# Kernel optimization log

Hardware: AMD Instinct MI355X
Metric: run time of the kernel (lower is better)

## Reference

```python
import jax, jax.numpy as jnp
import numpy as np

B, H, W, C = 4, 56, 56, 128
HEADS, KS, DEPTH, DEPTH_CROSS = 4, 7, 2, 2
HID = 4 * C
EPS = 1e-5


def layer_norm(x, g, b):
    m = jnp.mean(x, axis=-1, keepdims=True)
    v = jnp.mean((x - m) ** 2, axis=-1, keepdims=True)
    return (x - m) * jax.lax.rsqrt(v + EPS) * g + b


def _nbr_idx(L, k):
    # clamped sliding-window start (NATTEN semantics)
    s = np.clip(np.arange(L) - k // 2, 0, L - k)
    n = s[:, None] + np.arange(k)            # [L,k] neighbor coords
    r = n - np.arange(L)[:, None] + (k - 1)  # [L,k] rpb index in [0, 2k-2]
    return jnp.asarray(n), jnp.asarray(r)


def neighborhood_attention(q, kx, vx, rpb):
    # q,kx,vx: [B,h,H,W,d]; rpb: [h,2k-1,2k-1]
    b, h, hh, ww, d = q.shape
    k = KS
    ni, ri = _nbr_idx(hh, k)
    nj, rj = _nbr_idx(ww, k)
    q = q * (d ** -0.5)

    def gather(t):
        t = jnp.take(t, ni.reshape(-1), axis=2).reshape(b, h, hh, k, ww, d)
        t = jnp.take(t, nj.reshape(-1), axis=4).reshape(b, h, hh, k, ww, k, d)
        return t.transpose(0, 1, 2, 4, 3, 5, 6)  # [B,h,H,W,k,k,d]

    kn = gather(kx)
    vn = gather(vx)
    attn = jnp.einsum('bnhwd,bnhwijd->bnhwij', q, kn)
    bias = rpb[:, ri][:, :, :, rj]          # [h,H,k,W,k]
    bias = bias.transpose(0, 1, 3, 2, 4)     # [h,H,W,k,k]
    attn = attn + bias[None]
    attn = jax.nn.softmax(attn.reshape(b, h, hh, ww, k * k), axis=-1)
    out = jnp.einsum('bnhwm,bnhwmd->bnhwd', attn,
                     vn.reshape(b, h, hh, ww, k * k, d))
    return out.transpose(0, 2, 3, 1, 4).reshape(b, hh, ww, h * d)


def mlp(x, f1w, f1b, f2w, f2b):
    return jax.nn.gelu(x @ f1w + f1b, approximate=False) @ f2w + f2b


def sa_layer(x, n1g, n1b, qkvw, qkvb, rpb, pw, pb, n2g, n2b, f1w, f1b, f2w, f2b):
    b, hh, ww, c = x.shape
    d = c // HEADS
    hn = layer_norm(x, n1g, n1b)
    qkv = (hn @ qkvw + qkvb).reshape(b, hh, ww, 3, HEADS, d).transpose(3, 0, 4, 1, 2, 5)
    a = neighborhood_attention(qkv[0], qkv[1], qkv[2], rpb) @ pw + pb
    x = x + a
    x = x + mlp(layer_norm(x, n2g, n2b), f1w, f1b, f2w, f2b)
    return x


def cross_layer(x_multi, q_in, n1g, n1b, qw, qb, kvw, kvb, rpb, pw, pb,
                n2g, n2b, f1w, f1b, f2w, f2b):
    b, hh, ww, c = x_multi.shape
    d = c // HEADS
    hn = layer_norm(x_multi, n1g, n1b)
    q = (q_in @ qw + qb).reshape(b, hh, ww, HEADS, d).transpose(0, 3, 1, 2, 4)
    kv = (hn @ kvw + kvb).reshape(b, hh, ww, 2, HEADS, d).transpose(3, 0, 4, 1, 2, 5)
    a = neighborhood_attention(q, kv[0], kv[1], rpb) @ pw + pb
    x = x_multi + a
    x = x + mlp(layer_norm(x, n2g, n2b), f1w, f1b, f2w, f2b)
    return x


def setup_inputs() -> dict:
    key = jax.random.key(0)
    ks = iter(jax.random.split(key, 64))

    def nrm(shape, s=0.02):
        return (jax.random.normal(next(ks), shape, dtype=jnp.float32) * s)

    D, Dc = DEPTH, DEPTH_CROSS
    inp = {
        'x': jax.random.normal(next(ks), (B, H, W, C), dtype=jnp.float32),
        'x_multi': jax.random.normal(next(ks), (B, H, W, C), dtype=jnp.float32),
        # self-attention NATLayers (stacked over depth)
        'sa_n1g': jnp.ones((D, C), jnp.float32), 'sa_n1b': jnp.zeros((D, C), jnp.float32),
        'sa_qkv_w': nrm((D, C, 3 * C)), 'sa_qkv_b': jnp.zeros((D, 3 * C), jnp.float32),
        'sa_rpb': nrm((D, HEADS, 2 * KS - 1, 2 * KS - 1)),
        'sa_proj_w': nrm((D, C, C)), 'sa_proj_b': jnp.zeros((D, C), jnp.float32),
        'sa_n2g': jnp.ones((D, C), jnp.float32), 'sa_n2b': jnp.zeros((D, C), jnp.float32),
        'sa_fc1_w': nrm((D, C, HID)), 'sa_fc1_b': jnp.zeros((D, HID), jnp.float32),
        'sa_fc2_w': nrm((D, HID, C)), 'sa_fc2_b': jnp.zeros((D, C), jnp.float32),
        # cross NATCrossLayers (stacked over depth_cross)
        'cr_n1g': jnp.ones((Dc, C), jnp.float32), 'cr_n1b': jnp.zeros((Dc, C), jnp.float32),
        'cr_q_w': nrm((Dc, C, C)), 'cr_q_b': jnp.zeros((Dc, C), jnp.float32),
        'cr_kv_w': nrm((Dc, C, 2 * C)), 'cr_kv_b': jnp.zeros((Dc, 2 * C), jnp.float32),
        'cr_rpb': nrm((Dc, HEADS, 2 * KS - 1, 2 * KS - 1)),
        'cr_proj_w': nrm((Dc, C, C)), 'cr_proj_b': jnp.zeros((Dc, C), jnp.float32),
        'cr_n2g': jnp.ones((Dc, C), jnp.float32), 'cr_n2b': jnp.zeros((Dc, C), jnp.float32),
        'cr_fc1_w': nrm((Dc, C, HID)), 'cr_fc1_b': jnp.zeros((Dc, HID), jnp.float32),
        'cr_fc2_w': nrm((Dc, HID, C)), 'cr_fc2_b': jnp.zeros((Dc, C), jnp.float32),
        # downsample: conv (2C -> 4C, 3x3, stride 2, no bias) + LayerNorm
        'ds_conv_w': nrm((3, 3, 2 * C, 4 * C)),
        'ds_ng': jnp.ones((4 * C,), jnp.float32), 'ds_nb': jnp.zeros((4 * C,), jnp.float32),
    }
    return inp


def reference(x, x_multi,
              sa_n1g, sa_n1b, sa_qkv_w, sa_qkv_b, sa_rpb, sa_proj_w, sa_proj_b,
              sa_n2g, sa_n2b, sa_fc1_w, sa_fc1_b, sa_fc2_w, sa_fc2_b,
              cr_n1g, cr_n1b, cr_q_w, cr_q_b, cr_kv_w, cr_kv_b, cr_rpb,
              cr_proj_w, cr_proj_b, cr_n2g, cr_n2b, cr_fc1_w, cr_fc1_b,
              cr_fc2_w, cr_fc2_b, ds_conv_w, ds_ng, ds_nb):
    x_cross = x
    for i in range(DEPTH):
        x = sa_layer(x, sa_n1g[i], sa_n1b[i], sa_qkv_w[i], sa_qkv_b[i], sa_rpb[i],
                     sa_proj_w[i], sa_proj_b[i], sa_n2g[i], sa_n2b[i],
                     sa_fc1_w[i], sa_fc1_b[i], sa_fc2_w[i], sa_fc2_b[i])
    for i in range(DEPTH_CROSS):
        x_cross = cross_layer(x_multi, x_cross, cr_n1g[i], cr_n1b[i], cr_q_w[i],
                              cr_q_b[i], cr_kv_w[i], cr_kv_b[i], cr_rpb[i],
                              cr_proj_w[i], cr_proj_b[i], cr_n2g[i], cr_n2b[i],
                              cr_fc1_w[i], cr_fc1_b[i], cr_fc2_w[i], cr_fc2_b[i])
    y = jnp.concatenate([x, x_cross], axis=-1)  # [B,H,W,2C]
    y = jax.lax.conv_general_dilated(y, ds_conv_w, (2, 2), [(1, 1), (1, 1)],
                                     dimension_numbers=('NHWC', 'HWIO', 'NHWC'))
    return layer_norm(y, ds_ng, ds_nb)  # [B,H/2,W/2,4C]
```

## Files before the change

kernel.cpp:

```cpp
#include <hip/hip_runtime.h>
#include <math.h>

#define NPIX 12544
#define CH   128
#define HEADS 4
#define HD   32
#define KS   7
#define HID  512
#define HH   56
#define WW   56

typedef __attribute__((ext_vector_type(8))) short bf16x8;
typedef __attribute__((ext_vector_type(4))) float f32x4;
typedef unsigned short u16;

__device__ inline float gelu_f(float x) { return 0.5f * x * (1.0f + erff(x * 0.70710678118654752f)); }

__device__ inline u16 rne_bf16(float x) {
    unsigned u = __float_as_uint(x);
    return (u16)((u + 0x7fffu + ((u >> 16) & 1u)) >> 16);
}
__device__ inline float bf2f(u16 u) {
    return __uint_as_float(((unsigned)u) << 16);
}


template<int MODE>
__device__ __forceinline__ void qln_body(char* sh,
    const float* __restrict__ Af, const u16* __restrict__ Bt,
    const float* __restrict__ lng, const float* __restrict__ lnb,
    const float* __restrict__ bias, u16* __restrict__ Cb,
    int N, int bx, int by)
{
    char* alsb = sh;
    char* blsb = sh + 16384;
    int t = threadIdx.x, lane = t & 63, w = t >> 6;
    int m0 = bx * 64, n0 = by * 64;
    int wr = w >> 1, wc = w & 1;

    {
        int rb = t >> 3, c8 = t & 7;
        float4 va[2][4];
        float sum[2], sq[2];
#pragma unroll
        for (int r2 = 0; r2 < 2; ++r2) {
            int row = r2 * 32 + rb;
            const float4* ap = reinterpret_cast<const float4*>(Af + (size_t)(m0 + row) * 128);
            va[r2][0] = ap[c8 * 2];
            va[r2][1] = ap[c8 * 2 + 1];
            va[r2][2] = ap[16 + c8 * 2];
            va[r2][3] = ap[16 + c8 * 2 + 1];
            float s = 0.f, q = 0.f;
#pragma unroll
            for (int e = 0; e < 4; ++e) {
                float4 x = va[r2][e];
                s += x.x + x.y + x.z + x.w;
                q += x.x * x.x + x.y * x.y + x.z * x.z + x.w * x.w;
            }
            sum[r2] = s; sq[r2] = q;
        }
#pragma unroll
        for (int o = 1; o < 8; o <<= 1) {
            sum[0] += __shfl_xor(sum[0], o); sq[0] += __shfl_xor(sq[0], o);
            sum[1] += __shfl_xor(sum[1], o); sq[1] += __shfl_xor(sq[1], o);
        }
        const float4* gp = reinterpret_cast<const float4*>(lng);
        const float4* bp = reinterpret_cast<const float4*>(lnb);
        float4 g[4], bb[4];
        g[0] = gp[c8 * 2];      g[1] = gp[c8 * 2 + 1];
        g[2] = gp[16 + c8 * 2]; g[3] = gp[16 + c8 * 2 + 1];
        bb[0] = bp[c8 * 2];      bb[1] = bp[c8 * 2 + 1];
        bb[2] = bp[16 + c8 * 2]; bb[3] = bp[16 + c8 * 2 + 1];
#pragma unroll
        for (int r2 = 0; r2 < 2; ++r2) {
            int row = r2 * 32 + rb;
            float mean = sum[r2] * (1.0f / 128.0f);
            float inv = rsqrtf(sq[r2] * (1.0f / 128.0f) - mean * mean + 1e-5f);
#pragma unroll
            for (int h = 0; h < 2; ++h) {
                float4 x0 = va[r2][h * 2], x1 = va[r2][h * 2 + 1];
                float4 g0 = g[h * 2], g1 = g[h * 2 + 1];
                float4 b0 = bb[h * 2], b1 = bb[h * 2 + 1];
                bf16x8 o;
                o[0] = (short)rne_bf16((x0.x - mean) * inv * g0.x + b0.x);
                o[1] = (short)rne_bf16((x0.y - mean) * inv * g0.y + b0.y);
                o[2] = (short)rne_bf16((x0.z - mean) * inv * g0.z + b0.z);
                o[3] = (short)rne_bf16((x0.w - mean) * inv * g0.w + b0.w);
                o[4] = (short)rne_bf16((x1.x - mean) * inv * g1.x + b1.x);
                o[5] = (short)rne_bf16((x1.y - mean) * inv * g1.y + b1.y);
                o[6] = (short)rne_bf16((x1.z - mean) * inv * g1.z + b1.z);
                o[7] = (short)rne_bf16((x1.w - mean) * inv * g1.w + b1.w);
                int byte = (h * 128 + c8 * 16) ^ ((row & 7) << 4);
                *reinterpret_cast<bf16x8*>(alsb + row * 256 + byte) = o;
            }
        }
    }

    f32x4 acc[2][2] = {};
    for (int kk = 0; kk < 2; ++kk) {
#pragma unroll
        for (int i = 0; i < 2; ++i) {
            int s = t + i * 256, row = s >> 3, ch = (s & 7) * 8;
            bf16x8 v = *reinterpret_cast<const bf16x8*>(Bt + (size_t)(n0 + row) * 128 + kk * 64 + ch);
            *reinterpret_cast<bf16x8*>(blsb + row * 128 + ((ch * 2) ^ ((row & 7) << 4))) = v;
        }
        __syncthreads();
#pragma unroll
        for (int sub = 0; sub < 2; ++sub) {
            int kba = (kk * 2 + sub) * 64 + (lane >> 4) * 16;
            int kbb = sub * 64 + (lane >> 4) * 16;
            bf16x8 af[2], bfr[2];
#pragma unroll
            for (int mi = 0; mi < 2; ++mi) {
                int row = wr * 32 + mi * 16 + (lane & 15);
                af[mi] = *reinterpret_cast<const bf16x8*>(alsb + row * 256 + (kba ^ ((row & 7) << 4)));
            }
#pragma unroll
            for (int ni = 0; ni < 2; ++ni) {
                int row = wc * 32 + ni * 16 + (lane & 15);
                bfr[ni] = *reinterpret_cast<const bf16x8*>(blsb + row * 128 + (kbb ^ ((row & 7) << 4)));
            }
#pragma unroll
            for (int mi = 0; mi < 2; ++mi)
#pragma unroll
                for (int ni = 0; ni < 2; ++ni)
                    acc[mi][ni] = __builtin_amdgcn_mfma_f32_16x16x32_bf16(af[mi], bfr[ni], acc[mi][ni], 0, 0, 0);
        }
        __syncthreads();
    }

    int fq = lane >> 4, fr = lane & 15;
#pragma unroll
    for (int mi = 0; mi < 2; ++mi) {
#pragma unroll
        for (int ni = 0; ni < 2; ++ni) {
            int col = n0 + wc * 32 + ni * 16 + fr;
            float bv = bias[col];
#pragma unroll
            for (int j = 0; j < 4; ++j) {
                int row = m0 + wr * 32 + mi * 16 + fq * 4 + j;
                float v = acc[mi][ni][j] + bv;
                if constexpr (MODE == 1) {
                    Cb[(size_t)row * N + col] = rne_bf16(gelu_f(v));
                } else {
                    Cb[(size_t)row * N + col] = rne_bf16(v);
                }
            }
        }
    }
}

template<int MODE>
__device__ __forceinline__ void gemm_body(char* sh,
    const u16* __restrict__ A, const u16* __restrict__ Bt,
    const float* __restrict__ bias, const float* __restrict__ res,
    float* __restrict__ Cf, u16* __restrict__ Cb,
    int N, int K, int bx, int by)
{
    char* alsb = sh;
    char* blsb = sh + 4096;
    int t = threadIdx.x;
    int m0 = bx * 32, n0 = by * 64;
    int lane = t & 63, w = t >> 6;
    int wr = w >> 1, wc = w & 1;
    f32x4 acc[2] = {};
    for (int k0 = 0; k0 < K; k0 += 64) {
        {
            int s = t, row = s >> 3, ch = (s & 7) * 8;
            bf16x8 v = *reinterpret_cast<const bf16x8*>(A + (size_t)(m0 + row) * K + k0 + ch);
            *reinterpret_cast<bf16x8*>(alsb + row * 128 + ((ch * 2) ^ ((row & 7) << 4))) = v;
        }
#pragma unroll
        for (int i = 0; i < 2; ++i) {
            int s = t + i * 256, row = s >> 3, ch = (s & 7) * 8;
            bf16x8 v = *reinterpret_cast<const bf16x8*>(Bt + (size_t)(n0 + row) * K + k0 + ch);
            *reinterpret_cast<bf16x8*>(blsb + row * 128 + ((ch * 2) ^ ((row & 7) << 4))) = v;
        }
        __syncthreads();
#pragma unroll
        for (int kk = 0; kk < 2; ++kk) {
            int kb = kk * 64 + (lane >> 4) * 16;
            int row_a = wr * 16 + (lane & 15);
            bf16x8 af = *reinterpret_cast<const bf16x8*>(alsb + row_a * 128 + (kb ^ ((row_a & 7) << 4)));
#pragma unroll
            for (int ni = 0; ni < 2; ++ni) {
                int row = wc * 32 + ni * 16 + (lane & 15);
                bf16x8 bfr = *reinterpret_cast<const bf16x8*>(blsb + row * 128 + (kb ^ ((row & 7) << 4)));
                acc[ni] = __builtin_amdgcn_mfma_f32_16x16x32_bf16(af, bfr, acc[ni], 0, 0, 0);
            }
        }
        __syncthreads();
    }
    int fq = lane >> 4, fr = lane & 15;
#pragma unroll
    for (int ni = 0; ni < 2; ++ni) {
        int col = n0 + wc * 32 + ni * 16 + fr;
        float bv = bias[col];
#pragma unroll
        for (int j = 0; j < 4; ++j) {
            int row = m0 + wr * 16 + fq * 4 + j;
            float v = acc[ni][j] + bv;
            if constexpr (MODE == 2) {
                Cf[(size_t)row * N + col] = v + res[(size_t)row * N + col];
            } else if constexpr (MODE == 3) {
                Cb[(size_t)row * N + col] = rne_bf16(v);
            } else {
                float r2 = v + res[(size_t)row * N + col];
                Cf[(size_t)row * N + col] = r2;
                Cb[(size_t)row * N + col] = rne_bf16(r2);
            }
        }
    }
}


struct TDesc { const float* src; u16* dst; int K; int N; int tile0; };
struct TPack { TDesc d[19]; };

__global__ __launch_bounds__(256) void prep_kernel(TPack p, int ntile,
    const float* __restrict__ X, float* __restrict__ o1, float* __restrict__ o2,
    u16* __restrict__ ob, int n4)
{
    __shared__ float tl[32][33];
    if ((int)blockIdx.x < ntile) {
        int tile = blockIdx.x;
        int i = 0;
#pragma unroll 1
        while (i < 18 && tile >= p.d[i + 1].tile0) ++i;
        TDesc d = p.d[i];
        int local = tile - d.tile0;
        int ktiles = d.K >> 5;
        int lk = local % ktiles, ln_ = local / ktiles;
        int k0 = lk * 32, n0 = ln_ * 32;
        int tx = threadIdx.x & 31, ty = threadIdx.x >> 5;
#pragma unroll
        for (int r = 0; r < 4; ++r) {
            int row = ty * 4 + r;
            tl[row][tx] = d.src[(size_t)(k0 + row) * d.N + n0 + tx];
        }
        __syncthreads();
#pragma unroll
        for (int r = 0; r < 4; ++r) {
            int row = ty * 4 + r;
            d.dst[(size_t)(n0 + row) * d.K + k0 + tx] = rne_bf16(tl[tx][row]);
        }
    } else {
        int i = ((int)blockIdx.x - ntile) * 256 + threadIdx.x;
        if (i < n4) {
            float4 v = reinterpret_cast<const float4*>(X)[i];
            reinterpret_cast<float4*>(o1)[i] = v;
            reinterpret_cast<float4*>(o2)[i] = v;
            ushort4 o;
            o.x = rne_bf16(v.x); o.y = rne_bf16(v.y); o.z = rne_bf16(v.z); o.w = rne_bf16(v.w);
            reinterpret_cast<ushort4*>(ob)[i] = o;
        }
    }
}

__global__ __launch_bounds__(256) void stage1_kernel(
    const float* xb, const u16* qkvt, const float* n1g, const float* n1b, const float* qkvbias, u16* qkvout,
    const u16* xq, const u16* qwt, const float* qbias, u16* qout,
    const float* xm, const u16* kvt, const float* kn1g, const float* kn1b, const float* kvbias, u16* kvout)
{
    __shared__ __align__(16) char sh[24576];
    int b = blockIdx.x;
    if (b < 1176) {
        qln_body<3>(sh, xb, qkvt, n1g, n1b, qkvbias, qkvout, 384, b / 6, b % 6);
    } else if (b < 1960) {
        int lb = b - 1176;
        gemm_body<3>(sh, xq, qwt, qbias, nullptr, nullptr, qout, 128, 128, lb >> 1, lb & 1);
    } else {
        int lb = b - 1960;
        qln_body<3>(sh, xm, kvt, kn1g, kn1b, kvbias, kvout, 256, lb >> 2, lb & 3);
    }
}

__global__ __launch_bounds__(256) void proj_kernel(
    const u16* Asa, const u16* Bsa, const float* bsa, const float* rsa, float* Csa,
    const u16* Acr, const u16* Bcr, const float* bcr, const float* rcr, float* Ccr)
{
    __shared__ __align__(16) char sh[12288];
    if (blockIdx.x < 392)
        gemm_body<2>(sh, Asa, Bsa, bsa, rsa, Csa, nullptr, 128, 128, blockIdx.x, blockIdx.y);
    else
        gemm_body<2>(sh, Acr, Bcr, bcr, rcr, Ccr, nullptr, 128, 128, blockIdx.x - 392, blockIdx.y);
}

__global__ __launch_bounds__(256) void fc1_kernel(
    const float* Asa, const u16* Bsa, const float* g1, const float* b1, const float* bisa, u16* Csa,
    const float* Acr, const u16* Bcr, const float* g2, const float* b2, const float* bicr, u16* Ccr)
{
    __shared__ __align__(16) char sh[24576];
    if (blockIdx.x < 196)
        qln_body<1>(sh, Asa, Bsa, g1, b1, bisa, Csa, 512, blockIdx.x, blockIdx.y);
    else
        qln_body<1>(sh, Acr, Bcr, g2, b2, bicr, Ccr, 512, blockIdx.x - 196, blockIdx.y);
}

__global__ __launch_bounds__(256) void fc2_kernel(
    const u16* Asa, const u16* Bsa, const float* bsa, const float* rsa, float* Cfsa, u16* Cbsa,
    const u16* Acr, const u16* Bcr, const float* bcr, const float* rcr, float* Cfcr, u16* Cbcr)
{
    __shared__ __align__(16) char sh[12288];
    if (blockIdx.x < 392)
        gemm_body<4>(sh, Asa, Bsa, bsa, rsa, Cfsa, Cbsa, 128, 512, blockIdx.x, blockIdx.y);
    else
        gemm_body<4>(sh, Acr, Bcr, bcr, rcr, Cfcr, Cbcr, 128, 512, blockIdx.x - 392, blockIdx.y);
}

__global__ __launch_bounds__(256) void conv_mfma_kernel(
    const u16* __restrict__ Xb, const u16* __restrict__ Xc,
    const u16* __restrict__ Wt, float* __restrict__ Out)
{
    __shared__ u16 Als[32 * 64];
    __shared__ u16 Bls[64 * 64];
    char* alsb = reinterpret_cast<char*>(Als);
    char* blsb = reinterpret_cast<char*>(Bls);
    int t = threadIdx.x;
    int m0 = blockIdx.x * 32, n0 = blockIdx.y * 64;
    int lane = t & 63, w = t >> 6, wr = w >> 1, wc = w & 1;

    int arow = t >> 3, ach = (t & 7) * 8;
    int pm = m0 + arow;
    int b = pm / 784; int rem = pm - b * 784;
    int oi = rem / 28, oj = rem - oi * 28;
    int pb = b * 56, ib = 2 * oi - 1, jb = 2 * oj - 1;

    f32x4 acc[2] = {};
    for (int k0 = 0; k0 < 2304; k0 += 64) {
        {
            int k = k0 + ach;
            int tap = k >> 8, c = k & 255;
            int ky = (tap * 11) >> 5, kx = tap - ky * 3;
            int ii = ib + ky, jj = jb + kx;
            bf16x8 v = {};
            if ((unsigned)ii < 56u && (unsigned)jj < 56u) {
                const u16* src = (c < 128) ? Xb : Xc;
                v = *reinterpret_cast<const bf16x8*>(src + (size_t)((pb + ii) * 56 + jj) * 128 + (c & 127));
            }
            *reinterpret_cast<bf16x8*>(alsb + arow * 128 + ((ach * 2) ^ ((arow & 7) << 4))) = v;
        }
#pragma unroll
        for (int i = 0; i < 2; ++i) {
            int s = t + i * 256, row = s >> 3, ch = (s & 7) * 8;
            bf16x8 v = *reinterpret_cast<const bf16x8*>(Wt + (size_t)(n0 + row) * 2304 + k0 + ch);
            *reinterpret_cast<bf16x8*>(blsb + row * 128 + ((ch * 2) ^ ((row & 7) << 4))) = v;
        }
        __syncthreads();
#pragma unroll
        for (int kk = 0; kk < 2; ++kk) {
            int kb = kk * 64 + (lane >> 4) * 16;
            int row_a = wr * 16 + (lane & 15);
            bf16x8 af = *reinterpret_cast<const bf16x8*>(alsb + row_a * 128 + (kb ^ ((row_a & 7) << 4)));
#pragma unroll
            for (int ni = 0; ni < 2; ++ni) {
                int row = wc * 32 + ni * 16 + (lane & 15);
                bf16x8 bfr = *reinterpret_cast<const bf16x8*>(blsb + row * 128 + (kb ^ ((row & 7) << 4)));
                acc[ni] = __builtin_amdgcn_mfma_f32_16x16x32_bf16(af, bfr, acc[ni], 0, 0, 0);
            }
        }
        __syncthreads();
    }
    int fq = lane >> 4, fr = lane & 15;
#pragma unroll
    for (int ni = 0; ni < 2; ++ni) {
        int col = n0 + wc * 32 + ni * 16 + fr;
#pragma unroll
        for (int j = 0; j < 4; ++j) {
            int row = m0 + wr * 16 + fq * 4 + j;
            Out[(size_t)row * 512 + col] = acc[ni][j];
        }
    }
}

__global__ __launch_bounds__(256) void na2_kernel(
    const u16* __restrict__ Qa, int qlda, const u16* __restrict__ Ka, const u16* __restrict__ Va,
    int kvlda, const float* __restrict__ rpba, u16* __restrict__ Outa,
    const u16* __restrict__ Qb, int qldb, const u16* __restrict__ Kb, const u16* __restrict__ Vb,
    int kvldb, const float* __restrict__ rpbb, u16* __restrict__ Outb)
{
    __shared__ u16 KSls[144 * 40];
    __shared__ u16 Pls[32 * 168];
    __shared__ u16 Vtls[32 * 168];
    u16* Kls = KSls;
    u16* Sls16 = KSls;
    float* rls = reinterpret_cast<float*>(KSls + 4864);

    int sel = blockIdx.y >> 2;
    const u16* Q  = sel ? Qb : Qa;     int qld  = sel ? qldb : qlda;
    const u16* Kx = sel ? Kb : Ka;     const u16* Vx = sel ? Vb : Va;
    int kvld = sel ? kvldb : kvlda;
    const float* rpb = sel ? rpbb : rpba;
    u16* Out = sel ? Outb : Outa;
    int h = blockIdx.y & 3;

    int t = threadIdx.x, lane = t & 63, w = t >> 6;
    int blk = blockIdx.x;
    int b = blk / 98; int rem = blk - b * 98;
    int ti = rem / 7, tj = rem - ti * 7;
    int i0 = ti * 4, j0 = tj * 8;
    int r0 = min(max(i0 - 3, 0), 46), c0 = min(max(j0 - 3, 0), 42);
    int gbase = (b * 56 + r0) * 56 + c0;

    bf16x8 aq[2];
#pragma unroll
    for (int qt = 0; qt < 2; ++qt) {
        int q = qt * 16 + (lane & 15);
        int qi = q >> 3, qj = q & 7;
        aq[qt] = *reinterpret_cast<const bf16x8*>(
            Q + (size_t)((b * 56 + i0 + qi) * 56 + j0 + qj) * qld + h * 32 + (lane >> 4) * 8);
    }

    {
        uint4 z4 = make_uint4(0, 0, 0, 0);
        for (int i = t; i < 672; i += 256) reinterpret_cast<uint4*>(Pls)[i] = z4;
        if (t < 224) {
            int r = t / 7, k = t - r * 7;
            ushort4 z2; z2.x = 0; z2.y = 0; z2.z = 0; z2.w = 0;
            *reinterpret_cast<ushort4*>(Vtls + r * 168 + 140 + k * 4) = z2;
        }
    }

    for (int idx = t; idx < 280; idx += 256) {
        int pr2 = idx >> 2, c8 = (idx & 3) * 8;
        int p0 = pr2 * 2, p1 = p0 + 1;
        int ur0 = p0 / 14, uc0 = p0 - ur0 * 14;
        int ur1 = p1 / 14, uc1 = p1 - ur1 * 14;
        size_t g0 = (size_t)(gbase + ur0 * 56 + uc0) * kvld + h * 32 + c8;
        size_t g1 = (size_t)(gbase + ur1 * 56 + uc1) * kvld + h * 32 + c8;
        *reinterpret_cast<bf16x8*>(Kls + p0 * 40 + c8) = *reinterpret_cast<const bf16x8*>(Kx + g0);
        *reinterpret_cast<bf16x8*>(Kls + p1 * 40 + c8) = *reinterpret_cast<const bf16x8*>(Kx + g1);
        bf16x8 v0 = *reinterpret_cast<const bf16x8*>(Vx + g0);
        bf16x8 v1 = *reinterpret_cast<const bf16x8*>(Vx + g1);
#pragma unroll
        for (int e = 0; e < 8; ++e) {
            ushort2 pr; pr.x = (u16)v0[e]; pr.y = (u16)v1[e];
            *reinterpret_cast<ushort2*>(Vtls + (c8 + e) * 168 + p0) = pr;
        }
    }
    if (t < 16) {
        int r = 140 + (t >> 2), c8 = (t & 3) * 8;
        bf16x8 z8 = {};
        *reinterpret_cast<bf16x8*>(Kls + r * 40 + c8) = z8;
    }
    __syncthreads();

    f32x4 sacc[3][2] = {};
#pragma unroll
    for (int pi = 0; pi < 3; ++pi) {
        int pt = w + pi * 4;
        if (pt < 9) {
            bf16x8 bfrag = *reinterpret_cast<const bf16x8*>(Kls + (pt * 16 + (lane & 15)) * 40 + (lane >> 4) * 8);
#pragma unroll
            for (int qt = 0; qt < 2; ++qt)
                sacc[pi][qt] = __builtin_amdgcn_mfma_f32_16x16x32_bf16(aq[qt], bfrag, sacc[pi][qt], 0, 0, 0);
        }
    }
    __syncthreads();
#pragma unroll
    for (int pi = 0; pi < 3; ++pi) {
        int pt = w + pi * 4;
        if (pt < 9) {
#pragma unroll
            for (int qt = 0; qt < 2; ++qt) {
                int p = pt * 16 + (lane & 15), qr = qt * 16 + (lane >> 4) * 4;
#pragma unroll
                for (int j = 0; j < 4; ++j) Sls16[(qr + j) * 152 + p] = rne_bf16(sacc[pi][qt][j]);
            }
        }
    }
    if (t < 169) rls[t] = rpb[h * 169 + t];
    __syncthreads();

    int ai = lane / 7, aj = lane - ai * 7;
    for (int qq = 0; qq < 8; ++qq) {
        int q = w * 8 + qq;
        int qi = q >> 3, qj = q & 7;
        int i = i0 + qi, j = j0 + qj;
        int si = min(max(i - 3, 0), 49), sj = min(max(j - 3, 0), 49);
        int pu_base = (si - r0) * 14 + (sj - c0);
        float s = -1e30f; int pu = 0;
        if (lane < 49) {
            pu = pu_base + ai * 14 + aj;
            s = bf2f(Sls16[q * 152 + pu]) * 0.17677669529663687f
              + rls[(si - i + 6 + ai) * 13 + (sj - j + 6 + aj)];
        }
        float m = s;
#pragma unroll
        for (int o = 32; o > 0; o >>= 1) m = fmaxf(m, __shfl_xor(m, o));
        float e = (lane < 49) ? expf(s - m) : 0.f;
        float sum = e;
#pragma unroll
        for (int o = 32; o > 0; o >>= 1) sum += __shfl_xor(sum, o);
        if (lane < 49) Pls[q * 168 + pu] = rne_bf16(e / sum);
    }
    __syncthreads();

    int qt = w >> 1, ct = w & 1;
    f32x4 oacc = {};
#pragma unroll
    for (int k = 0; k < 5; ++k) {
        bf16x8 pa = *reinterpret_cast<const bf16x8*>(Pls + (qt * 16 + (lane & 15)) * 168 + k * 32 + (lane >> 4) * 8);
        bf16x8 vb = *reinterpret_cast<const bf16x8*>(Vtls + (ct * 16 + (lane & 15)) * 168 + k * 32 + (lane >> 4) * 8);
        oacc = __builtin_amdgcn_mfma_f32_16x16x32_bf16(pa, vb, oacc, 0, 0, 0);
    }
    int ch = ct * 16 + (lane & 15);
#pragma unroll
    for (int j = 0; j < 4; ++j) {
        int q = qt * 16 + (lane >> 4) * 4 + j;
        int qi = q >> 3, qj = q & 7;
        Out[(size_t)((b * 56 + i0 + qi) * 56 + j0 + qj) * CH + h * 32 + ch] = rne_bf16(oacc[j]);
    }
}

__global__ __launch_bounds__(256) void ln512_out_kernel(const float* __restrict__ in,
    const float* __restrict__ g, const float* __restrict__ b, float* __restrict__ out)
{
    int w = threadIdx.x >> 6, lane = threadIdx.x & 63;
    int p = blockIdx.x * 4 + w;
    const float4* ip = reinterpret_cast<const float4*>(in + (size_t)p * 512);
    float4 v0 = ip[lane * 2], v1 = ip[lane * 2 + 1];
    float vals[8] = { v0.x, v0.y, v0.z, v0.w, v1.x, v1.y, v1.z, v1.w };
    float s = 0.f, sq = 0.f;
#pragma unroll
    for (int q = 0; q < 8; ++q) { s += vals[q]; sq += vals[q] * vals[q]; }
#pragma unroll
    for (int o = 32; o > 0; o >>= 1) { s += __shfl_xor(s, o); sq += __shfl_xor(sq, o); }
    float mean = s * (1.0f / 512.0f);
    float inv = rsqrtf(sq * (1.0f / 512.0f) - mean * mean + 1e-5f);
#pragma unroll
    for (int q = 0; q < 8; ++q) {
        int c = lane * 8 + q;
        out[(size_t)p * 512 + c] = (vals[q] - mean) * inv * g[c] + b[c];
    }
}

extern "C" void kernel_launch(void* const* d_in, const int* in_sizes, int n_in,
                              void* d_out, int out_size, void* d_ws, size_t ws_size,
                              hipStream_t stream)
{
    const float* X      = (const float*)d_in[0];
    const float* XM     = (const float*)d_in[1];
    const float* sa_n1g = (const float*)d_in[2];
    const float* sa_n1b = (const float*)d_in[3];
    const float* sa_qkvw= (const float*)d_in[4];
    const float* sa_qkvb= (const float*)d_in[5];
    const float* sa_rpb = (const float*)d_in[6];
    const float* sa_pw  = (const float*)d_in[7];
    const float* sa_pb  = (const float*)d_in[8];
    const float* sa_n2g = (const float*)d_in[9];
    const float* sa_n2b = (const float*)d_in[10];
    const float* sa_f1w = (const float*)d_in[11];
    const float* sa_f1b = (const float*)d_in[12];
    const float* sa_f2w = (const float*)d_in[13];
    const float* sa_f2b = (const float*)d_in[14];
    const float* cr_n1g = (const float*)d_in[15];
    const float* cr_n1b = (const float*)d_in[16];
    const float* cr_qw  = (const float*)d_in[17];
    const float* cr_qb  = (const float*)d_in[18];
    const float* cr_kvw = (const float*)d_in[19];
    const float* cr_kvb = (const float*)d_in[20];
    const float* cr_rpb = (const float*)d_in[21];
    const float* cr_pw  = (const float*)d_in[22];
    const float* cr_pb  = (const float*)d_in[23];
    const float* cr_n2g = (const float*)d_in[24];
    const float* cr_n2b = (const float*)d_in[25];
    const float* cr_f1w = (const float*)d_in[26];
    const float* cr_f1b = (const float*)d_in[27];
    const float* cr_f2w = (const float*)d_in[28];
    const float* cr_f2b = (const float*)d_in[29];
    const float* dconvw = (const float*)d_in[30];
    const float* ds_ng  = (const float*)d_in[31];
    const float* ds_nb  = (const float*)d_in[32];

    const size_t NC = (size_t)NPIX * CH;
    float* ws   = (float*)d_ws;
    float* xb   = ws;
    float* xcb  = xb + NC;
    float* bigR = xcb + NC;
    u16* bigb   = (u16*)bigR;
    u16* hnb    = (u16*)(bigR + 2 * NC);
    u16* attnb  = hnb + NC;
    u16* xcbbf  = attnb + NC;
    u16* xbbf   = xcbbf + NC;
    u16* qkvb   = xbbf + NC;
    u16* bufQb  = qkvb + (size_t)NPIX * 384;
    u16* wa     = bufQb + NC;
    u16* kvb    = bigb;
    u16* bigcr  = qkvb;

    TPack tp;
    int tile = 0, idx = 0;
    u16* p = wa;
    u16* qkvt[2]; u16* pwt[2]; u16* f1t[2]; u16* f2t[2];
    u16* qt[2];   u16* kvt[2]; u16* cpt[2]; u16* cf1t[2];
    u16* cf2t[2]; u16* convt;
    auto add = [&](const float* s, u16*& dst, int K, int N) {
        dst = p;
        tp.d[idx].src = s; tp.d[idx].dst = p; tp.d[idx].K = K; tp.d[idx].N = N; tp.d[idx].tile0 = tile;
        tile += (K / 32) * (N / 32); p += (size_t)K * N; ++idx;
    };
    for (int l = 0; l < 2; ++l) add(sa_qkvw + (size_t)l * 128 * 384, qkvt[l], 128, 384);
    for (int l = 0; l < 2; ++l) add(sa_pw   + (size_t)l * 128 * 128, pwt[l],  128, 128);
    for (int l = 0; l < 2; ++l) add(sa_f1w  + (size_t)l * 128 * 512, f1t[l],  128, 512);
    for (int l = 0; l < 2; ++l) add(sa_f2w  + (size_t)l * 512 * 128, f2t[l],  512, 128);
    for (int l = 0; l < 2; ++l) add(cr_qw   + (size_t)l * 128 * 128, qt[l],   128, 128);
    for (int l = 0; l < 2; ++l) add(cr_kvw  + (size_t)l * 128 * 256, kvt[l],  128, 256);
    for (int l = 0; l < 2; ++l) add(cr_pw   + (size_t)l * 128 * 128, cpt[l],  128, 128);
    for (int l = 0; l < 2; ++l) add(cr_f1w  + (size_t)l * 128 * 512, cf1t[l], 128, 512);
    for (int l = 0; l < 2; ++l) add(cr_f2w  + (size_t)l * 512 * 128, cf2t[l], 512, 128);
    add(dconvw, convt, 2304, 512);

    const int n4 = NPIX * CH / 4;
    const int ndup = (n4 + 255) / 256;
    prep_kernel<<<tile + ndup, 256, 0, stream>>>(tp, tile, X, xb, xcb, xcbbf, n4);

    for (int l = 0; l < 2; ++l) {
        stage1_kernel<<<2744, 256, 0, stream>>>(
            xb, qkvt[l], sa_n1g + l * CH, sa_n1b + l * CH, sa_qkvb + l * 384, qkvb,
            xcbbf, qt[l], cr_qb + l * CH, bufQb,
            XM, kvt[l], cr_n1g + l * CH, cr_n1b + l * CH, cr_kvb + l * 256, kvb);
        na2_kernel<<<dim3(392, 8), 256, 0, stream>>>(
            qkvb, 384, qkvb + 128, qkvb + 256, 384, sa_rpb + l * HEADS * 169, attnb,
            bufQb, 128, kvb, kvb + 128, 256, cr_rpb + l * HEADS * 169, hnb);
        proj_kernel<<<dim3(784, 2), 256, 0, stream>>>(
            attnb, pwt[l], sa_pb + l * CH, xb, xb,
            hnb, cpt[l], cr_pb + l * CH, XM, xcb);
        fc1_kernel<<<dim3(392, 8), 256, 0, stream>>>(
            xb, f1t[l], sa_n2g + l * CH, sa_n2b + l * CH, sa_f1b + l * HID, bigb,
            xcb, cf1t[l], cr_n2g + l * CH, cr_n2b + l * CH, cr_f1b + l * HID, bigcr);
        fc2_kernel<<<dim3(784, 2), 256, 0, stream>>>(
            bigb, f2t[l], sa_f2b + l * CH, xb, xb, xbbf,
            bigcr, cf2t[l], cr_f2b + l * CH, xcb, xcb, xcbbf);
    }

    conv_mfma_kernel<<<dim3(3136 / 32, 512 / 64), 256, 0, stream>>>(xbbf, xcbbf, convt, bigR);
    ln512_out_kernel<<<3136 / 4, 256, 0, stream>>>(bigR, ds_ng, ds_nb, (float*)d_out);
}
```

Before: 233.2 us.

## Fuse LN, FC1, GELU and FC2 into one MLP kernel per 32-row tile

Replaces the separate fc1 and fc2 launches with a single mlp_kernel. Each block layer-norms 32 rows, computes the 512-wide GELU hidden activations into LDS, and then runs FC2 plus the residual add directly from LDS. This removes the global write and re-read of the bf16 hidden tensor and one launch per layer. In exchange it uses 48KB of LDS per block, launches only 784 blocks, serialises small per-iteration weight loads with syncs, and gets little MFMA work per sync.

```diff
diff --git a/kernel.cpp b/kernel.cpp
--- a/kernel.cpp
+++ b/kernel.cpp
@@ -202,12 +202,126 @@
             float v = acc[ni][j] + bv;
             if constexpr (MODE == 2) {
                 Cf[(size_t)row * N + col] = v + res[(size_t)row * N + col];
-            } else if constexpr (MODE == 3) {
+            } else {
                 Cb[(size_t)row * N + col] = rne_bf16(v);
-            } else {
-                float r2 = v + res[(size_t)row * N + col];
-                Cf[(size_t)row * N + col] = r2;
-                Cb[(size_t)row * N + col] = rne_bf16(r2);
+            }
+        }
+    }
+}
+
+__device__ __forceinline__ void mlp_body(char* sh,
+    float* __restrict__ Xs, const u16* __restrict__ F1, const u16* __restrict__ F2,
+    const float* __restrict__ lng, const float* __restrict__ lnb,
+    const float* __restrict__ b1, const float* __restrict__ b2,
+    u16* __restrict__ Mb, int bx)
+{
+    char* als = sh;
+    char* hls = sh + 8192;
+    char* bls = sh + 40960;
+    int t = threadIdx.x, lane = t & 63, w = t >> 6;
+    int m0 = bx * 32;
+    int fq = lane >> 4, fr = lane & 15;
+    int mh = w >> 1, nh = w & 1;
+
+    {
+        int row = t >> 3, c8 = t & 7;
+        const float4* ap = reinterpret_cast<const float4*>(Xs + (size_t)(m0 + row) * 128 + c8 * 16);
+        float4 v[4] = { ap[0], ap[1], ap[2], ap[3] };
+        float s = 0.f, q = 0.f;
+#pragma unroll
+        for (int e = 0; e < 4; ++e) {
+            s += v[e].x + v[e].y + v[e].z + v[e].w;
+            q += v[e].x * v[e].x + v[e].y * v[e].y + v[e].z * v[e].z + v[e].w * v[e].w;
+        }
+#pragma unroll
+        for (int o = 1; o < 8; o <<= 1) { s += __shfl_xor(s, o); q += __shfl_xor(q, o); }
+        float mean = s * (1.0f / 128.0f);
+        float inv = rsqrtf(q * (1.0f / 128.0f) - mean * mean + 1e-5f);
+        const float4* gp = reinterpret_cast<const float4*>(lng + c8 * 16);
+        const float4* bp = reinterpret_cast<const float4*>(lnb + c8 * 16);
+#pragma unroll
+        for (int h2 = 0; h2 < 2; ++h2) {
+            float4 x0 = v[h2 * 2], x1 = v[h2 * 2 + 1];
+            float4 g0 = gp[h2 * 2], g1 = gp[h2 * 2 + 1];
+            float4 b0 = bp[h2 * 2], b1v = bp[h2 * 2 + 1];
+            bf16x8 o;
+            o[0] = (short)rne_bf16((x0.x - mean) * inv * g0.x + b0.x);
+            o[1] = (short)rne_bf16((x0.y - mean) * inv * g0.y + b0.y);
+            o[2] = (short)rne_bf16((x0.z - mean) * inv * g0.z + b0.z);
+            o[3] = (short)rne_bf16((x0.w - mean) * inv * g0.w + b0.w);
+            o[4] = (short)rne_bf16((x1.x - mean) * inv * g1.x + b1v.x);
+            o[5] = (short)rne_bf16((x1.y - mean) * inv * g1.y + b1v.y);
+            o[6] = (short)rne_bf16((x1.z - mean) * inv * g1.z + b1v.z);
+            o[7] = (short)rne_bf16((x1.w - mean) * inv * g1.w + b1v.w);
+            int byte = (c8 * 32 + h2 * 16) ^ ((row & 7) << 4);
+            *reinterpret_cast<bf16x8*>(als + row * 256 + byte) = o;
+        }
+    }
+
+    for (int ny = 0; ny < 16; ++ny) {
+#pragma unroll
+        for (int i = 0; i < 2; ++i) {
+            int s = t + i * 256, brow = s >> 4, c = s & 15;
+            bf16x8 v = *reinterpret_cast<const bf16x8*>(F1 + (size_t)(ny * 32 + brow) * 128 + c * 8);
+            *reinterpret_cast<bf16x8*>(bls + brow * 256 + ((c * 16) ^ ((brow & 7) << 4))) = v;
+        }
+        __syncthreads();
+        f32x4 a = {};
+#pragma unroll
+        for (int kc = 0; kc < 4; ++kc) {
+            int kb = kc * 64 + fq * 16;
+            int ar = mh * 16 + fr;
+            bf16x8 af = *reinterpret_cast<const bf16x8*>(als + ar * 256 + (kb ^ ((ar & 7) << 4)));
+            int br = nh * 16 + fr;
+            bf16x8 bf = *reinterpret_cast<const bf16x8*>(bls + br * 256 + (kb ^ ((br & 7) << 4)));
+            a = __builtin_amdgcn_mfma_f32_16x16x32_bf16(af, bf, a, 0, 0, 0);
+        }
+        int col = ny * 32 + nh * 16 + fr;
+        float bv = b1[col];
+#pragma unroll
+        for (int j = 0; j < 4; ++j) {
+            int r = mh * 16 + fq * 4 + j;
+            *reinterpret_cast<u16*>(hls + r * 1024 + ((col * 2) ^ ((r & 7) << 4))) = rne_bf16(gelu_f(a[j] + bv));
+        }
+        __syncthreads();
+    }
+
+#pragma unroll 1
+    for (int oc = 0; oc < 2; ++oc) {
+        f32x4 a2[2] = {};
+        for (int ks = 0; ks < 8; ++ks) {
+#pragma unroll
+            for (int i = 0; i < 2; ++i) {
+                int s = t + i * 256, brow = s >> 3, c = s & 7;
+                bf16x8 v = *reinterpret_cast<const bf16x8*>(F2 + (size_t)(oc * 64 + brow) * 512 + ks * 64 + c * 8);
+                *reinterpret_cast<bf16x8*>(bls + brow * 128 + ((c * 16) ^ ((brow & 7) << 4))) = v;
+            }
+            __syncthreads();
+#pragma unroll
+            for (int kk = 0; kk < 2; ++kk) {
+                int ar = mh * 16 + fr;
+                int hkb = ks * 128 + kk * 64 + fq * 16;
+                bf16x8 af = *reinterpret_cast<const bf16x8*>(hls + ar * 1024 + (hkb ^ ((ar & 7) << 4)));
+                int bkb = kk * 64 + fq * 16;
+#pragma unroll
+                for (int ni = 0; ni < 2; ++ni) {
+                    int br = nh * 32 + ni * 16 + fr;
+                    bf16x8 bf = *reinterpret_cast<const bf16x8*>(bls + br * 128 + (bkb ^ ((br & 7) << 4)));
+                    a2[ni] = __builtin_amdgcn_mfma_f32_16x16x32_bf16(af, bf, a2[ni], 0, 0, 0);
+                }
+            }
+            __syncthreads();
+        }
+#pragma unroll
+        for (int ni = 0; ni < 2; ++ni) {
+            int col = oc * 64 + nh * 32 + ni * 16 + fr;
+            float bv = b2[col];
+#pragma unroll
+            for (int j = 0; j < 4; ++j) {
+                int row = m0 + mh * 16 + fq * 4 + j;
+                float r2 = a2[ni][j] + bv + Xs[(size_t)row * 128 + col];
+                Xs[(size_t)row * 128 + col] = r2;
+                Mb[(size_t)row * 128 + col] = rne_bf16(r2);
             }
         }
     }
@@ -286,26 +400,17 @@
         gemm_body<2>(sh, Acr, Bcr, bcr, rcr, Ccr, nullptr, 128, 128, blockIdx.x - 392, blockIdx.y);
 }
 
-__global__ __launch_bounds__(256) void fc1_kernel(
-    const float* Asa, const u16* Bsa, const float* g1, const float* b1, const float* bisa, u16* Csa,
-    const float* Acr, const u16* Bcr, const float* g2, const float* b2, const float* bicr, u16* Ccr)
-{
-    __shared__ __align__(16) char sh[24576];
-    if (blockIdx.x < 196)
-        qln_body<1>(sh, Asa, Bsa, g1, b1, bisa, Csa, 512, blockIdx.x, blockIdx.y);
+__global__ __launch_bounds__(256) void mlp_kernel(
+    float* Xsa, const u16* F1sa, const u16* F2sa, const float* gsa, const float* bsa,
+    const float* b1sa, const float* b2sa, u16* Msa,
+    float* Xcr, const u16* F1cr, const u16* F2cr, const float* gcr, const float* bcr,
+    const float* b1cr, const float* b2cr, u16* Mcr)
+{
+    __shared__ __align__(16) char sh[49152];
+    if (blockIdx.x < 392)
+        mlp_body(sh, Xsa, F1sa, F2sa, gsa, bsa, b1sa, b2sa, Msa, blockIdx.x);
     else
-        qln_body<1>(sh, Acr, Bcr, g2, b2, bicr, Ccr, 512, blockIdx.x - 196, blockIdx.y);
-}
-
-__global__ __launch_bounds__(256) void fc2_kernel(
-    const u16* Asa, const u16* Bsa, const float* bsa, const float* rsa, float* Cfsa, u16* Cbsa,
-    const u16* Acr, const u16* Bcr, const float* bcr, const float* rcr, float* Cfcr, u16* Cbcr)
-{
-    __shared__ __align__(16) char sh[12288];
-    if (blockIdx.x < 392)
-        gemm_body<4>(sh, Asa, Bsa, bsa, rsa, Cfsa, Cbsa, 128, 512, blockIdx.x, blockIdx.y);
-    else
-        gemm_body<4>(sh, Acr, Bcr, bcr, rcr, Cfcr, Cbcr, 128, 512, blockIdx.x - 392, blockIdx.y);
+        mlp_body(sh, Xcr, F1cr, F2cr, gcr, bcr, b1cr, b2cr, Mcr, blockIdx.x - 392);
 }
 
 __global__ __launch_bounds__(256) void conv_mfma_kernel(
@@ -587,7 +692,6 @@
     u16* bufQb  = qkvb + (size_t)NPIX * 384;
     u16* wa     = bufQb + NC;
     u16* kvb    = bigb;
-    u16* bigcr  = qkvb;
 
     TPack tp;
     int tile = 0, idx = 0;
@@ -626,12 +730,11 @@
         proj_kernel<<<dim3(784, 2), 256, 0, stream>>>(
             attnb, pwt[l], sa_pb + l * CH, xb, xb,
             hnb, cpt[l], cr_pb + l * CH, XM, xcb);
-        fc1_kernel<<<dim3(392, 8), 256, 0, stream>>>(
-            xb, f1t[l], sa_n2g + l * CH, sa_n2b + l * CH, sa_f1b + l * HID, bigb,
-            xcb, cf1t[l], cr_n2g + l * CH, cr_n2b + l * CH, cr_f1b + l * HID, bigcr);
-        fc2_kernel<<<dim3(784, 2), 256, 0, stream>>>(
-            bigb, f2t[l], sa_f2b + l * CH, xb, xb, xbbf,
-            bigcr, cf2t[l], cr_f2b + l * CH, xcb, xcb, xcbbf);
+        mlp_kernel<<<784, 256, 0, stream>>>(
+            xb, f1t[l], f2t[l], sa_n2g + l * CH, sa_n2b + l * CH,
+            sa_f1b + l * HID, sa_f2b + l * CH, xbbf,
+            xcb, cf1t[l], cf2t[l], cr_n2g + l * CH, cr_n2b + l * CH,
+            cr_f1b + l * HID, cr_f2b + l * CH, xcbbf);
     }
 
     conv_mfma_kernel<<<dim3(3136 / 32, 512 / 64), 256, 0, stream>>>(xbbf, xcbbf, convt, bigR);
```

New measurement: 252.2 us. 8.2% more time.
